# Kernel tuning notes

Measured on AMD Instinct MI355X. Metric: run time of the kernel, lower is better.

The kernel has to match this reference:

```python
import jax, jax.numpy as jnp
import numpy as np
import math

N_HEAD = 16
K_SPARSE = 64

def setup_inputs() -> dict:
    key = jax.random.key(0)
    ks = jax.random.split(key, 12)
    B, T, C = 1, 2048, 1024
    s = 0.02
    return {
        "x":   jax.random.normal(ks[0], (B, T, C), jnp.float32),
        "Wq":  jax.random.normal(ks[1], (C, C), jnp.float32) * s,
        "bq":  jax.random.normal(ks[2], (C,), jnp.float32) * s,
        "Wk":  jax.random.normal(ks[3], (C, C), jnp.float32) * s,
        "bk":  jax.random.normal(ks[4], (C,), jnp.float32) * s,
        "Wv":  jax.random.normal(ks[5], (C, C), jnp.float32) * s,
        "bv":  jax.random.normal(ks[6], (C,), jnp.float32) * s,
        "Wo":  jax.random.normal(ks[7], (C, C), jnp.float32) * s,
        "bo":  jax.random.normal(ks[8], (C,), jnp.float32) * s,
        "Wks": jax.random.normal(ks[9], (C,), jnp.float32) * s,
        "bks": jax.random.normal(ks[10], (), jnp.float32) * s,
    }

def reference(x, Wq, bq, Wk, bk, Wv, bv, Wo, bo, Wks, bks):
    B, T, C = x.shape
    nh = N_HEAD
    hs = C // nh
    k_val = min(K_SPARSE, T)

    # projections -> (B, nh, T, hs)   (torch Linear: x @ W.T + b)
    q = (x @ Wq.T + bq).reshape(B, T, nh, hs).transpose(0, 2, 1, 3)
    k = (x @ Wk.T + bk).reshape(B, T, nh, hs).transpose(0, 2, 1, 3)
    v = (x @ Wv.T + bv).reshape(B, T, nh, hs).transpose(0, 2, 1, 3)

    # key scorer: per-token scalar score (B, T)
    key_scores = x @ Wks + bks

    # causal masking of scores, then per-query top-k key selection
    pos = jnp.arange(T)
    causal = pos[None, :] <= pos[:, None]                      # (T, T), True where key<=query
    masked = jnp.where(causal[None], key_scores[:, None, :], -jnp.inf)  # (B, T, T)
    _, top_k_idx = jax.lax.top_k(masked, k_val)                # (B, T, k)
    top_k_idx = jnp.minimum(top_k_idx, pos[None, :, None])     # clamp to <= query pos

    # gather sparse keys/values: (B, nh, T, k, hs)
    bi = jnp.arange(B)[:, None, None, None]
    hi = jnp.arange(nh)[None, :, None, None]
    gi = top_k_idx[:, None, :, :]                              # (B, 1, T, k)
    sparse_k = k[bi, hi, gi]                                   # (B, nh, T, k, hs)
    sparse_v = v[bi, hi, gi]

    scale = 1.0 / math.sqrt(hs)
    logits = jnp.einsum('bhtd,bhtkd->bhtk', q, sparse_k) * scale
    probs = jax.nn.softmax(logits, axis=-1)
    out = jnp.einsum('bhtk,bhtkd->bhtd', probs, sparse_v)      # (B, nh, T, hs)
    out = out.transpose(0, 2, 1, 3).reshape(B, T, C)
    return out @ Wo.T + bo
```

## Files before the change

### kernel.cpp

```cpp
#include <hip/hip_runtime.h>
#include <hip/hip_bf16.h>
#include <cstdint>
#include <cstddef>

#define T_DIM 2048
#define C_DIM 1024
#define NH 16
#define HS 64
#define KSP 64

#define GBM 128
#define GBN 64
#define GBK 128
#define OBM 64
#define OBN 64

#define ATB 16
#define USLOT (KSP + ATB - 1)
#define KSTR 66

#define DPP_XOR1 0xB1
#define DPP_XOR2 0x4E
#define DPP_HMIRR 0x141
#define DPP_ROR8 0x128

typedef short short8 __attribute__((ext_vector_type(8)));
typedef float f32x4 __attribute__((ext_vector_type(4)));
typedef _Float16 half2_t __attribute__((ext_vector_type(2)));

__device__ __forceinline__ unsigned short f2bfu(float f) {
  unsigned u = __builtin_bit_cast(unsigned, f);
  unsigned r = (u + 0x7fffu + ((u >> 16) & 1u)) >> 16;
  return (unsigned short)r;
}
__device__ __forceinline__ unsigned short f2h(float f) {
  _Float16 h = (_Float16)f;
  return __builtin_bit_cast(unsigned short, h);
}
__device__ __forceinline__ float bflo(unsigned u) {
  return __builtin_bit_cast(float, u << 16);
}
__device__ __forceinline__ float bfhi(unsigned u) {
  return __builtin_bit_cast(float, u & 0xffff0000u);
}

template <int CTRL>
__device__ __forceinline__ float dpp_add_f(float x) {
  const int xi = __builtin_bit_cast(int, x);
  const int y = __builtin_amdgcn_update_dpp(xi, xi, CTRL, 0xF, 0xF, true);
  return x + __builtin_bit_cast(float, y);
}
template <int CTRL>
__device__ __forceinline__ float dpp_max_f(float x) {
  const int xi = __builtin_bit_cast(int, x);
  const int y = __builtin_amdgcn_update_dpp(xi, xi, CTRL, 0xF, 0xF, true);
  return fmaxf(x, __builtin_bit_cast(float, y));
}

__device__ __forceinline__ float dot2h(unsigned kbits, unsigned qbits, float acc) {
#if __has_builtin(__builtin_amdgcn_fdot2)
  return __builtin_amdgcn_fdot2(__builtin_bit_cast(half2_t, kbits),
                                __builtin_bit_cast(half2_t, qbits), acc, false);
#else
  half2_t kk = __builtin_bit_cast(half2_t, kbits);
  half2_t qq = __builtin_bit_cast(half2_t, qbits);
  return acc + (float)kk.x * (float)qq.x + (float)kk.y * (float)qq.y;
#endif
}

#define GLOAD_LDS16(gp, lp)                                                  \
  __builtin_amdgcn_global_load_lds(                                          \
      (const __attribute__((address_space(1))) void*)(gp),                   \
      (__attribute__((address_space(3))) void*)(lp), 16, 0, 0)

#define NSCORE (T_DIM / 4)
#define NCONV ((T_DIM * C_DIM + 4 * C_DIM * C_DIM) / 4 / 256)
__global__ __launch_bounds__(256) void convert_scores_kernel(
    const float* __restrict__ x, const float* __restrict__ Wq,
    const float* __restrict__ Wk, const float* __restrict__ Wv,
    const float* __restrict__ Wo, const float* __restrict__ Wks,
    const float* __restrict__ bks,
    unsigned short* __restrict__ xb, unsigned short* __restrict__ Wqb,
    unsigned short* __restrict__ Wkb, unsigned short* __restrict__ Wvb,
    unsigned short* __restrict__ Wob, float* __restrict__ scores) {
  if (blockIdx.x < NSCORE) {
    const int t = blockIdx.x * 4 + (threadIdx.x >> 6);
    const int lane = threadIdx.x & 63;
    const float* xrow = x + (size_t)t * C_DIM;
    float acc = 0.f;
    #pragma unroll 4
    for (int i = lane; i < C_DIM; i += 64)
      acc += xrow[i] * Wks[i];
    #pragma unroll
    for (int o = 32; o; o >>= 1) acc += __shfl_xor(acc, o);
    if (lane == 0) scores[t] = acc + bks[0];
    return;
  }
  const int i = (blockIdx.x - NSCORE) * 256 + threadIdx.x;
  const int NX4 = T_DIM * C_DIM / 4;
  const int NW4 = C_DIM * C_DIM / 4;
  const float* src;
  unsigned short* dst;
  int j = i;
  if (j < NX4) { src = x; dst = xb; }
  else {
    j -= NX4;
    int w = j / NW4;
    j -= w * NW4;
    src = (w == 0) ? Wq : (w == 1) ? Wk : (w == 2) ? Wv : Wo;
    dst = (w == 0) ? Wqb : (w == 1) ? Wkb : (w == 2) ? Wvb : Wob;
  }
  float4 f = reinterpret_cast<const float4*>(src)[j];
  ushort4 o;
  o.x = f2bfu(f.x); o.y = f2bfu(f.y); o.z = f2bfu(f.z); o.w = f2bfu(f.w);
  reinterpret_cast<ushort4*>(dst)[j] = o;
}

__device__ __forceinline__ void gemm_body_128x64(
    const unsigned short* __restrict__ A, const unsigned short* __restrict__ W,
    f32x4 acc[4][2], int bm, int bn, int tid,
    unsigned short* As, unsigned short* Ws) {
  const int w = tid >> 6, lane = tid & 63;
  const int quad = lane >> 4, r = lane & 15;
  const int wm = (w >> 1) * 64, wn = (w & 1) * 32;
  const int sub = lane >> 4;
  const int c = lane & 15;
  const unsigned short* Arow[8];
  const unsigned short* Wrow[4];
  #pragma unroll
  for (int i = 0; i < 8; ++i) {
    const int row = w * 32 + i * 4 + sub;
    Arow[i] = A + (size_t)(bm * GBM + row) * C_DIM + ((c ^ (row & 7)) * 8);
  }
  #pragma unroll
  for (int i = 0; i < 4; ++i) {
    const int row = w * 16 + i * 4 + sub;
    Wrow[i] = W + (size_t)(bn * GBN + row) * C_DIM + ((c ^ (row & 7)) * 8);
  }
  for (int kb = 0; kb < C_DIM; kb += GBK) {
    #pragma unroll
    for (int i = 0; i < 8; ++i)
      GLOAD_LDS16(Arow[i] + kb, &As[(w * 32 + i * 4) * GBK]);
    #pragma unroll
    for (int i = 0; i < 4; ++i)
      GLOAD_LDS16(Wrow[i] + kb, &Ws[(w * 16 + i * 4) * GBK]);
    __syncthreads();
    #pragma unroll
    for (int ks = 0; ks < 4; ++ks) {
      const int pc = ((ks * 4 + quad) ^ (r & 7)) * 8;
      short8 af[4], bfr[2];
      #pragma unroll
      for (int mi = 0; mi < 4; ++mi)
        af[mi] = *reinterpret_cast<const short8*>(&As[(wm + mi * 16 + r) * GBK + pc]);
      #pragma unroll
      for (int ni = 0; ni < 2; ++ni)
        bfr[ni] = *reinterpret_cast<const short8*>(&Ws[(wn + ni * 16 + r) * GBK + pc]);
      #pragma unroll
      for (int mi = 0; mi < 4; ++mi)
        #pragma unroll
        for (int ni = 0; ni < 2; ++ni)
          acc[mi][ni] = __builtin_amdgcn_mfma_f32_16x16x32_bf16(af[mi], bfr[ni], acc[mi][ni], 0, 0, 0);
    }
    __syncthreads();
  }
}

#define NRANK (T_DIM / 4)
__global__ __launch_bounds__(256) void gemm_qkv_rank_kernel(
    const unsigned short* __restrict__ A,
    const unsigned short* __restrict__ Wq, const unsigned short* __restrict__ Wk,
    const unsigned short* __restrict__ Wv,
    const float* __restrict__ bq, const float* __restrict__ bk,
    const float* __restrict__ bv,
    unsigned short* __restrict__ qo, unsigned short* __restrict__ ko,
    unsigned short* __restrict__ vo,
    const float* __restrict__ scores, int* __restrict__ sorted_idx) {
  __shared__ unsigned short lds[(GBM + GBN) * GBK];
  const int tid = threadIdx.x;
  if (blockIdx.x < NRANK) {
    float* ss = reinterpret_cast<float*>(lds);
    for (int j = tid; j < T_DIM; j += 256) ss[j] = scores[j];
    __syncthreads();
    const int w = tid >> 6, lane = tid & 63;
    const int i = blockIdx.x * 4 + w;
    const float si = ss[i];
    int rank = 0;
    #pragma unroll
    for (int step = 0; step < T_DIM / 64; ++step) {
      const int j = step * 64 + lane;
      const float sj = ss[j];
      rank += (int)((sj > si) || (sj == si && j < i));
    }
    #pragma unroll
    for (int o = 32; o; o >>= 1) rank += __shfl_xor(rank, o);
    if (lane == 0) sorted_idx[rank] = i;
    return;
  }
  const int bid = blockIdx.x - NRANK;
  const int per = (T_DIM / GBM) * (C_DIM / GBN);
  const int which = bid / per;
  const int rem = bid % per;
  const int bm = rem / (C_DIM / GBN);
  const int bn = rem % (C_DIM / GBN);
  const unsigned short* W = (which == 0) ? Wq : (which == 1) ? Wk : Wv;
  const float* bias = (which == 0) ? bq : (which == 1) ? bk : bv;
  unsigned short* out = (which == 0) ? qo : (which == 1) ? ko : vo;
  f32x4 acc[4][2] = {};
  gemm_body_128x64(A, W, acc, bm, bn, tid, lds, lds + GBM * GBK);
  const int w = tid >> 6, lane = tid & 63;
  const int quad = lane >> 4, r = lane & 15;
  const int wm = (w >> 1) * 64, wn = (w & 1) * 32;
  #pragma unroll
  for (int mi = 0; mi < 4; ++mi) {
    #pragma unroll
    for (int ni = 0; ni < 2; ++ni) {
      const int col = bn * GBN + wn + ni * 16 + r;
      const float bf = bias[col];
      #pragma unroll
      for (int i = 0; i < 4; ++i) {
        const int row = bm * GBM + wm + mi * 16 + quad * 4 + i;
        const float val = acc[mi][ni][i] + bf;
        out[(size_t)row * C_DIM + col] = (which == 2) ? f2bfu(val) : f2h(val);
      }
    }
  }
}

__device__ __forceinline__ void gemm_body_64x64(
    const unsigned short* __restrict__ A, const unsigned short* __restrict__ W,
    f32x4 acc[2][2], int bm, int bn, int tid) {
  __shared__ unsigned short As[OBM * GBK];
  __shared__ unsigned short Ws[OBN * GBK];
  const int w = tid >> 6, lane = tid & 63;
  const int quad = lane >> 4, r = lane & 15;
  const int wm = (w >> 1) * 32, wn = (w & 1) * 32;
  const int sub = lane >> 4;
  const int c = lane & 15;
  const unsigned short* Arow[4];
  const unsigned short* Wrow[4];
  #pragma unroll
  for (int i = 0; i < 4; ++i) {
    const int row = w * 16 + i * 4 + sub;
    Arow[i] = A + (size_t)(bm * OBM + row) * C_DIM + ((c ^ (row & 7)) * 8);
    Wrow[i] = W + (size_t)(bn * OBN + row) * C_DIM + ((c ^ (row & 7)) * 8);
  }
  for (int kb = 0; kb < C_DIM; kb += GBK) {
    #pragma unroll
    for (int i = 0; i < 4; ++i)
      GLOAD_LDS16(Arow[i] + kb, &As[(w * 16 + i * 4) * GBK]);
    #pragma unroll
    for (int i = 0; i < 4; ++i)
      GLOAD_LDS16(Wrow[i] + kb, &Ws[(w * 16 + i * 4) * GBK]);
    __syncthreads();
    #pragma unroll
    for (int ks = 0; ks < 4; ++ks) {
      const int pc = ((ks * 4 + quad) ^ (r & 7)) * 8;
      short8 af[2], bfr[2];
      #pragma unroll
      for (int mi = 0; mi < 2; ++mi)
        af[mi] = *reinterpret_cast<const short8*>(&As[(wm + mi * 16 + r) * GBK + pc]);
      #pragma unroll
      for (int ni = 0; ni < 2; ++ni)
        bfr[ni] = *reinterpret_cast<const short8*>(&Ws[(wn + ni * 16 + r) * GBK + pc]);
      #pragma unroll
      for (int mi = 0; mi < 2; ++mi)
        #pragma unroll
        for (int ni = 0; ni < 2; ++ni)
          acc[mi][ni] = __builtin_amdgcn_mfma_f32_16x16x32_bf16(af[mi], bfr[ni], acc[mi][ni], 0, 0, 0);
    }
    __syncthreads();
  }
}

__global__ __launch_bounds__(256) void gemm_o_f32_kernel(
    const unsigned short* __restrict__ A, const unsigned short* __restrict__ W,
    const float* __restrict__ bias, float* __restrict__ out) {
  const int tid = threadIdx.x;
  const int bm = blockIdx.x / (C_DIM / OBN);
  const int bn = blockIdx.x % (C_DIM / OBN);
  f32x4 acc[2][2] = {};
  gemm_body_64x64(A, W, acc, bm, bn, tid);
  const int w = tid >> 6, lane = tid & 63;
  const int quad = lane >> 4, r = lane & 15;
  const int wm = (w >> 1) * 32, wn = (w & 1) * 32;
  #pragma unroll
  for (int mi = 0; mi < 2; ++mi) {
    #pragma unroll
    for (int ni = 0; ni < 2; ++ni) {
      const int col = bn * OBN + wn + ni * 16 + r;
      const float bf = bias[col];
      #pragma unroll
      for (int i = 0; i < 4; ++i) {
        const int row = bm * OBM + wm + mi * 16 + quad * 4 + i;
        out[(size_t)row * C_DIM + col] = acc[mi][ni][i] + bf;
      }
    }
  }
}

__global__ __launch_bounds__(256) void select_kernel(
    const int* __restrict__ sorted_idx, unsigned short* __restrict__ sel) {
  const int tid = threadIdx.x;
  const int w = tid >> 6, lane = tid & 63;
  const int t = blockIdx.x * 4 + w;
  unsigned short* dst = sel + (size_t)t * KSP;
  if (t <= 63) {
    dst[lane] = (unsigned short)((lane < t) ? lane : t);
    return;
  }
  const unsigned long long lt_mask = (1ull << lane) - 1ull;
  int count = 0;
  for (int c = 0; c < T_DIM / 64 && count < KSP; ++c) {
    int s = sorted_idx[c * 64 + lane];
    s = (s < 0) ? 0 : (s > T_DIM - 1 ? T_DIM - 1 : s);
    const bool ok = (s <= t);
    const unsigned long long mm = __ballot(ok);
    const int pos = count + __popcll(mm & lt_mask);
    if (ok && pos < KSP) dst[pos] = (unsigned short)s;
    count += __popcll(mm);
  }
}

__global__ __launch_bounds__(256) void attn_kernel(
    const unsigned short* __restrict__ q, const unsigned short* __restrict__ k,
    const unsigned short* __restrict__ v, const unsigned short* __restrict__ sel,
    unsigned short* __restrict__ attn_out) {
  __shared__ unsigned short Kl[USLOT * KSTR];
  __shared__ unsigned short Vl[USLOT * KSTR];
  __shared__ short map_s[T_DIM];
  __shared__ short urows[USLOT];
  const int tb = blockIdx.x >> 4;
  const int h = blockIdx.x & (NH - 1);
  const int t0 = tb * ATB;
  const int tid = threadIdx.x;
  const int w = tid >> 6, lane = tid & 63;
  const int c8 = lane & 7;
  const int ksub = lane >> 3;
  uint4 qr[ATB / 4];
  #pragma unroll
  for (int li = 0; li < ATB / 4; ++li) {
    const int t = t0 + w * (ATB / 4) + li;
    qr[li] = *reinterpret_cast<const uint4*>(q + (size_t)t * C_DIM + h * HS + 8 * c8);
  }
  if (tid < KSP) {
    const int r0 = sel[(size_t)t0 * KSP + tid];
    map_s[r0] = (short)tid;
    urows[tid] = (short)r0;
  } else if (tid < USLOT) {
    const int row = t0 + 1 + (tid - KSP);
    map_s[row] = (short)tid;
    urows[tid] = (short)row;
  }
  __syncthreads();
  {
    const int e8 = tid & 7;
    for (int s = tid >> 3; s < USLOT; s += 32) {
      const int row = urows[s];
      const size_t gb = (size_t)row * C_DIM + h * HS + e8 * 8;
      *reinterpret_cast<uint4*>(&Kl[s * KSTR + e8 * 8]) =
          *reinterpret_cast<const uint4*>(k + gb);
      *reinterpret_cast<uint4*>(&Vl[s * KSTR + e8 * 8]) =
          *reinterpret_cast<const uint4*>(v + gb);
    }
  }
  __syncthreads();
  #pragma unroll 2
  for (int li = 0; li < ATB / 4; ++li) {
    const int tt = w * (ATB / 4) + li;
    const int t = t0 + tt;
    const uint4 qraw = qr[li];
    const unsigned short* __restrict__ selt = sel + (size_t)t * KSP;
    int slot[8];
    #pragma unroll
    for (int jj = 0; jj < 8; ++jj)
      slot[jj] = map_s[selt[8 * jj + ksub]];
    float l[8];
    #pragma unroll
    for (int jj = 0; jj < 8; ++jj) {
      const uint4 raw =
          *reinterpret_cast<const uint4*>(&Kl[slot[jj] * KSTR + 8 * c8]);
      float pl = dot2h(raw.x, qraw.x, 0.f);
      pl = dot2h(raw.y, qraw.y, pl);
      pl = dot2h(raw.z, qraw.z, pl);
      pl = dot2h(raw.w, qraw.w, pl);
      pl *= 0.125f;
      pl = dpp_add_f<DPP_XOR1>(pl);
      pl = dpp_add_f<DPP_XOR2>(pl);
      pl = dpp_add_f<DPP_HMIRR>(pl);
      l[jj] = pl;
    }
    float m = l[0];
    #pragma unroll
    for (int jj = 1; jj < 8; ++jj) m = fmaxf(m, l[jj]);
    m = dpp_max_f<DPP_ROR8>(m);
    m = fmaxf(m, __shfl_xor(m, 16));
    m = fmaxf(m, __shfl_xor(m, 32));
    float sum = 0.f;
    #pragma unroll
    for (int jj = 0; jj < 8; ++jj) {
      l[jj] = __expf(l[jj] - m);
      sum += l[jj];
    }
    sum = dpp_add_f<DPP_ROR8>(sum);
    sum += __shfl_xor(sum, 16);
    sum += __shfl_xor(sum, 32);
    const float rs = 1.0f / sum;
    float a[8] = {0.f, 0.f, 0.f, 0.f, 0.f, 0.f, 0.f, 0.f};
    #pragma unroll
    for (int jj = 0; jj < 8; ++jj) {
      const uint4 raw =
          *reinterpret_cast<const uint4*>(&Vl[slot[jj] * KSTR + 8 * c8]);
      const float p = l[jj] * rs;
      a[0] += p * bflo(raw.x); a[1] += p * bfhi(raw.x);
      a[2] += p * bflo(raw.y); a[3] += p * bfhi(raw.y);
      a[4] += p * bflo(raw.z); a[5] += p * bfhi(raw.z);
      a[6] += p * bflo(raw.w); a[7] += p * bfhi(raw.w);
    }
    #pragma unroll
    for (int z = 0; z < 8; ++z) a[z] = dpp_add_f<DPP_ROR8>(a[z]);
    #pragma unroll
    for (int z = 0; z < 8; ++z) a[z] += __shfl_xor(a[z], 16);
    #pragma unroll
    for (int z = 0; z < 8; ++z) a[z] += __shfl_xor(a[z], 32);
    if (ksub == 0) {
      ushort4 o0, o1;
      o0.x = f2bfu(a[0]); o0.y = f2bfu(a[1]); o0.z = f2bfu(a[2]); o0.w = f2bfu(a[3]);
      o1.x = f2bfu(a[4]); o1.y = f2bfu(a[5]); o1.z = f2bfu(a[6]); o1.w = f2bfu(a[7]);
      ushort4* dst =
          reinterpret_cast<ushort4*>(attn_out + (size_t)t * C_DIM + h * HS + 8 * c8);
      dst[0] = o0;
      dst[1] = o1;
    }
  }
}

extern "C" void kernel_launch(void* const* d_in, const int* in_sizes, int n_in,
                              void* d_out, int out_size, void* d_ws, size_t ws_size,
                              hipStream_t stream) {
  const float* x   = (const float*)d_in[0];
  const float* Wq  = (const float*)d_in[1];
  const float* bq  = (const float*)d_in[2];
  const float* Wk  = (const float*)d_in[3];
  const float* bk  = (const float*)d_in[4];
  const float* Wv  = (const float*)d_in[5];
  const float* bv  = (const float*)d_in[6];
  const float* Wo  = (const float*)d_in[7];
  const float* bo  = (const float*)d_in[8];
  const float* Wks = (const float*)d_in[9];
  const float* bks = (const float*)d_in[10];
  float* out = (float*)d_out;

  char* ws = (char*)d_ws;
  size_t off = 0;
  float* scores = (float*)(ws + off); off += 8192;
  int*   sorted = (int*)(ws + off);   off += 8192;
  unsigned short* selb = (unsigned short*)(ws + off); off += (size_t)T_DIM * KSP * 2;
  unsigned short* xb  = (unsigned short*)(ws + off); off += (size_t)T_DIM * C_DIM * 2;
  unsigned short* Wqb = (unsigned short*)(ws + off); off += (size_t)C_DIM * C_DIM * 2;
  unsigned short* Wkb = (unsigned short*)(ws + off); off += (size_t)C_DIM * C_DIM * 2;
  unsigned short* Wvb = (unsigned short*)(ws + off); off += (size_t)C_DIM * C_DIM * 2;
  unsigned short* Wob = (unsigned short*)(ws + off); off += (size_t)C_DIM * C_DIM * 2;
  unsigned short* qb  = (unsigned short*)(ws + off); off += (size_t)T_DIM * C_DIM * 2;
  unsigned short* kb  = (unsigned short*)(ws + off); off += (size_t)T_DIM * C_DIM * 2;
  unsigned short* vb  = (unsigned short*)(ws + off); off += (size_t)T_DIM * C_DIM * 2;
  unsigned short* ab  = xb;

  convert_scores_kernel<<<NSCORE + NCONV, 256, 0, stream>>>(
      x, Wq, Wk, Wv, Wo, Wks, bks, xb, Wqb, Wkb, Wvb, Wob, scores);

  gemm_qkv_rank_kernel<<<NRANK + 3 * (T_DIM / GBM) * (C_DIM / GBN), 256, 0,
                         stream>>>(
      xb, Wqb, Wkb, Wvb, bq, bk, bv, qb, kb, vb, scores, sorted);

  select_kernel<<<T_DIM / 4, 256, 0, stream>>>(sorted, selb);

  attn_kernel<<<(T_DIM / ATB) * NH, 256, 0, stream>>>(qb, kb, vb, selb, ab);

  gemm_o_f32_kernel<<<(T_DIM / OBM) * (C_DIM / OBN), 256, 0, stream>>>(
      ab, Wob, bo, out);
}
```

Before: 160.8 us.

## Compute sparse attention over shared key-row union with MFMA and multiplicity mask

Rewrites the attention kernel so each 16-query block scores all 80 candidate rows (the 64 keys selected for the block's first query plus the following rows) with 16x16x32 f16 MFMA instructions. A per-query count table adds log(multiplicity) to the logits of selected rows and masks unselected rows, so the softmax over the union equals the softmax over each query's own gathered keys. V is stored transposed in LDS so that P·V also runs on MFMA, and V becomes f16 instead of bf16. This replaces per-query gathered dot products, DPP reductions and scalar accumulation with matrix-core work, at the cost of scoring unselected rows and a count-table setup step. It relies on every query's selected keys falling inside that 80-row union.

```diff
diff --git a/kernel.cpp b/kernel.cpp
--- a/kernel.cpp
+++ b/kernel.cpp
@@ -16,17 +16,14 @@
 #define OBN 64
 
 #define ATB 16
-#define USLOT (KSP + ATB - 1)
-#define KSTR 66
-
-#define DPP_XOR1 0xB1
-#define DPP_XOR2 0x4E
-#define DPP_HMIRR 0x141
-#define DPP_ROR8 0x128
+#define KLS 72
+#define VTS 108
+#define PLS 104
+#define CNS 104
 
 typedef short short8 __attribute__((ext_vector_type(8)));
 typedef float f32x4 __attribute__((ext_vector_type(4)));
-typedef _Float16 half2_t __attribute__((ext_vector_type(2)));
+typedef _Float16 half8 __attribute__((ext_vector_type(8)));
 
 __device__ __forceinline__ unsigned short f2bfu(float f) {
   unsigned u = __builtin_bit_cast(unsigned, f);
@@ -36,36 +33,6 @@
 __device__ __forceinline__ unsigned short f2h(float f) {
   _Float16 h = (_Float16)f;
   return __builtin_bit_cast(unsigned short, h);
-}
-__device__ __forceinline__ float bflo(unsigned u) {
-  return __builtin_bit_cast(float, u << 16);
-}
-__device__ __forceinline__ float bfhi(unsigned u) {
-  return __builtin_bit_cast(float, u & 0xffff0000u);
-}
-
-template <int CTRL>
-__device__ __forceinline__ float dpp_add_f(float x) {
-  const int xi = __builtin_bit_cast(int, x);
-  const int y = __builtin_amdgcn_update_dpp(xi, xi, CTRL, 0xF, 0xF, true);
-  return x + __builtin_bit_cast(float, y);
-}
-template <int CTRL>
-__device__ __forceinline__ float dpp_max_f(float x) {
-  const int xi = __builtin_bit_cast(int, x);
-  const int y = __builtin_amdgcn_update_dpp(xi, xi, CTRL, 0xF, 0xF, true);
-  return fmaxf(x, __builtin_bit_cast(float, y));
-}
-
-__device__ __forceinline__ float dot2h(unsigned kbits, unsigned qbits, float acc) {
-#if __has_builtin(__builtin_amdgcn_fdot2)
-  return __builtin_amdgcn_fdot2(__builtin_bit_cast(half2_t, kbits),
-                                __builtin_bit_cast(half2_t, qbits), acc, false);
-#else
-  half2_t kk = __builtin_bit_cast(half2_t, kbits);
-  half2_t qq = __builtin_bit_cast(half2_t, qbits);
-  return acc + (float)kk.x * (float)qq.x + (float)kk.y * (float)qq.y;
-#endif
 }
 
 #define GLOAD_LDS16(gp, lp)                                                  \
@@ -220,7 +187,7 @@
       for (int i = 0; i < 4; ++i) {
         const int row = bm * GBM + wm + mi * 16 + quad * 4 + i;
         const float val = acc[mi][ni][i] + bf;
-        out[(size_t)row * C_DIM + col] = (which == 2) ? f2bfu(val) : f2h(val);
+        out[(size_t)row * C_DIM + col] = f2h(val);
       }
     }
   }
@@ -321,116 +288,167 @@
   }
 }
 
-__global__ __launch_bounds__(256) void attn_kernel(
+__global__ __launch_bounds__(128) void attn_kernel(
     const unsigned short* __restrict__ q, const unsigned short* __restrict__ k,
     const unsigned short* __restrict__ v, const unsigned short* __restrict__ sel,
     unsigned short* __restrict__ attn_out) {
-  __shared__ unsigned short Kl[USLOT * KSTR];
-  __shared__ unsigned short Vl[USLOT * KSTR];
+  __shared__ unsigned short Kl[2][80 * KLS];
+  __shared__ unsigned short Vt[2][64 * VTS];
+  __shared__ unsigned short Pl[2][16 * PLS];
+  __shared__ unsigned int   cnt[16 * CNS];
   __shared__ short map_s[T_DIM];
-  __shared__ short urows[USLOT];
-  const int tb = blockIdx.x >> 4;
-  const int h = blockIdx.x & (NH - 1);
+  __shared__ short urows[80];
+  const int tb = blockIdx.x >> 3;
+  const int hg = blockIdx.x & 7;
   const int t0 = tb * ATB;
   const int tid = threadIdx.x;
   const int w = tid >> 6, lane = tid & 63;
-  const int c8 = lane & 7;
-  const int ksub = lane >> 3;
-  uint4 qr[ATB / 4];
-  #pragma unroll
-  for (int li = 0; li < ATB / 4; ++li) {
-    const int t = t0 + w * (ATB / 4) + li;
-    qr[li] = *reinterpret_cast<const uint4*>(q + (size_t)t * C_DIM + h * HS + 8 * c8);
-  }
+  const int qd = lane >> 4;
+  const int r = lane & 15;
+  const int h = hg * 2 + w;
+
+  uint4 qf[2];
+  #pragma unroll
+  for (int kc = 0; kc < 2; ++kc)
+    qf[kc] = *reinterpret_cast<const uint4*>(
+        q + (size_t)(t0 + r) * C_DIM + h * HS + kc * 32 + qd * 8);
+
   if (tid < KSP) {
     const int r0 = sel[(size_t)t0 * KSP + tid];
     map_s[r0] = (short)tid;
     urows[tid] = (short)r0;
-  } else if (tid < USLOT) {
+  } else if (tid < 79) {
     const int row = t0 + 1 + (tid - KSP);
     map_s[row] = (short)tid;
     urows[tid] = (short)row;
-  }
+  } else if (tid == 79) {
+    urows[79] = (short)t0;
+  }
+  for (int i = tid; i < 16 * CNS; i += 128) cnt[i] = 0u;
   __syncthreads();
+
   {
-    const int e8 = tid & 7;
-    for (int s = tid >> 3; s < USLOT; s += 32) {
-      const int row = urows[s];
-      const size_t gb = (size_t)row * C_DIM + h * HS + e8 * 8;
-      *reinterpret_cast<uint4*>(&Kl[s * KSTR + e8 * 8]) =
-          *reinterpret_cast<const uint4*>(k + gb);
-      *reinterpret_cast<uint4*>(&Vl[s * KSTR + e8 * 8]) =
-          *reinterpret_cast<const uint4*>(v + gb);
+    const int e8 = lane & 7;
+    const int pr = lane >> 3;
+    #pragma unroll
+    for (int sb = 0; sb < 5; ++sb) {
+      const int s0 = sb * 16 + pr * 2;
+      const int row0 = urows[s0], row1 = urows[s0 + 1];
+      const size_t g0 = (size_t)row0 * C_DIM + h * HS + e8 * 8;
+      const size_t g1 = (size_t)row1 * C_DIM + h * HS + e8 * 8;
+      const uint4 k0 = *reinterpret_cast<const uint4*>(k + g0);
+      const uint4 k1 = *reinterpret_cast<const uint4*>(k + g1);
+      const uint4 v0 = *reinterpret_cast<const uint4*>(v + g0);
+      const uint4 v1 = *reinterpret_cast<const uint4*>(v + g1);
+      *reinterpret_cast<uint4*>(&Kl[w][s0 * KLS + ((e8 ^ (s0 & 7)) * 8)]) = k0;
+      *reinterpret_cast<uint4*>(&Kl[w][(s0 + 1) * KLS + ((e8 ^ ((s0 + 1) & 7)) * 8)]) = k1;
+      const unsigned* v0w = reinterpret_cast<const unsigned*>(&v0);
+      const unsigned* v1w = reinterpret_cast<const unsigned*>(&v1);
+      #pragma unroll
+      for (int dd = 0; dd < 8; ++dd) {
+        const unsigned lo = (v0w[dd >> 1] >> ((dd & 1) * 16)) & 0xffffu;
+        const unsigned hi = (v1w[dd >> 1] >> ((dd & 1) * 16)) & 0xffffu;
+        *reinterpret_cast<unsigned*>(&Vt[w][(e8 * 8 + dd) * VTS + s0]) =
+            lo | (hi << 16);
+      }
+    }
+    #pragma unroll
+    for (int z = 0; z < 4; ++z)
+      *reinterpret_cast<unsigned long long*>(&Vt[w][lane * VTS + 80 + z * 4]) = 0ull;
+    if (t0 < 64) {
+      #pragma unroll
+      for (int e = 0; e < 8; ++e) {
+        const int idx = tid + e * 128;
+        const int tl = idx >> 6;
+        const int rr = sel[(size_t)(t0 + tl) * KSP + (idx & 63)];
+        atomicAdd(&cnt[tl * CNS + map_s[rr]], 1u);
+      }
+    } else {
+      #pragma unroll
+      for (int e = 0; e < 8; ++e) {
+        const int idx = tid + e * 128;
+        const int tl = idx >> 6;
+        const int rr = sel[(size_t)(t0 + tl) * KSP + (idx & 63)];
+        cnt[tl * CNS + map_s[rr]] = 1u;
+      }
     }
   }
   __syncthreads();
-  #pragma unroll 2
-  for (int li = 0; li < ATB / 4; ++li) {
-    const int tt = w * (ATB / 4) + li;
-    const int t = t0 + tt;
-    const uint4 qraw = qr[li];
-    const unsigned short* __restrict__ selt = sel + (size_t)t * KSP;
-    int slot[8];
-    #pragma unroll
-    for (int jj = 0; jj < 8; ++jj)
-      slot[jj] = map_s[selt[8 * jj + ksub]];
-    float l[8];
-    #pragma unroll
-    for (int jj = 0; jj < 8; ++jj) {
-      const uint4 raw =
-          *reinterpret_cast<const uint4*>(&Kl[slot[jj] * KSTR + 8 * c8]);
-      float pl = dot2h(raw.x, qraw.x, 0.f);
-      pl = dot2h(raw.y, qraw.y, pl);
-      pl = dot2h(raw.z, qraw.z, pl);
-      pl = dot2h(raw.w, qraw.w, pl);
-      pl *= 0.125f;
-      pl = dpp_add_f<DPP_XOR1>(pl);
-      pl = dpp_add_f<DPP_XOR2>(pl);
-      pl = dpp_add_f<DPP_HMIRR>(pl);
-      l[jj] = pl;
-    }
-    float m = l[0];
-    #pragma unroll
-    for (int jj = 1; jj < 8; ++jj) m = fmaxf(m, l[jj]);
-    m = dpp_max_f<DPP_ROR8>(m);
-    m = fmaxf(m, __shfl_xor(m, 16));
-    m = fmaxf(m, __shfl_xor(m, 32));
-    float sum = 0.f;
-    #pragma unroll
-    for (int jj = 0; jj < 8; ++jj) {
-      l[jj] = __expf(l[jj] - m);
-      sum += l[jj];
-    }
-    sum = dpp_add_f<DPP_ROR8>(sum);
-    sum += __shfl_xor(sum, 16);
-    sum += __shfl_xor(sum, 32);
-    const float rs = 1.0f / sum;
-    float a[8] = {0.f, 0.f, 0.f, 0.f, 0.f, 0.f, 0.f, 0.f};
-    #pragma unroll
-    for (int jj = 0; jj < 8; ++jj) {
-      const uint4 raw =
-          *reinterpret_cast<const uint4*>(&Vl[slot[jj] * KSTR + 8 * c8]);
-      const float p = l[jj] * rs;
-      a[0] += p * bflo(raw.x); a[1] += p * bfhi(raw.x);
-      a[2] += p * bflo(raw.y); a[3] += p * bfhi(raw.y);
-      a[4] += p * bflo(raw.z); a[5] += p * bfhi(raw.z);
-      a[6] += p * bflo(raw.w); a[7] += p * bfhi(raw.w);
-    }
-    #pragma unroll
-    for (int z = 0; z < 8; ++z) a[z] = dpp_add_f<DPP_ROR8>(a[z]);
-    #pragma unroll
-    for (int z = 0; z < 8; ++z) a[z] += __shfl_xor(a[z], 16);
-    #pragma unroll
-    for (int z = 0; z < 8; ++z) a[z] += __shfl_xor(a[z], 32);
-    if (ksub == 0) {
-      ushort4 o0, o1;
-      o0.x = f2bfu(a[0]); o0.y = f2bfu(a[1]); o0.z = f2bfu(a[2]); o0.w = f2bfu(a[3]);
-      o1.x = f2bfu(a[4]); o1.y = f2bfu(a[5]); o1.z = f2bfu(a[6]); o1.w = f2bfu(a[7]);
-      ushort4* dst =
-          reinterpret_cast<ushort4*>(attn_out + (size_t)t * C_DIM + h * HS + 8 * c8);
-      dst[0] = o0;
-      dst[1] = o1;
-    }
+
+  f32x4 s5[5] = {};
+  #pragma unroll
+  for (int ut = 0; ut < 5; ++ut) {
+    #pragma unroll
+    for (int kc = 0; kc < 2; ++kc) {
+      const uint4 kw = *reinterpret_cast<const uint4*>(
+          &Kl[w][(ut * 16 + r) * KLS + (((kc * 4 + qd) ^ (r & 7)) * 8)]);
+      s5[ut] = __builtin_amdgcn_mfma_f32_16x16x32_f16(
+          __builtin_bit_cast(half8, kw), __builtin_bit_cast(half8, qf[kc]),
+          s5[ut], 0, 0, 0);
+    }
+  }
+  float mx = -3.0e38f;
+  #pragma unroll
+  for (int ut = 0; ut < 5; ++ut) {
+    const uint4 c4 = *reinterpret_cast<const uint4*>(&cnt[r * CNS + ut * 16 + qd * 4]);
+    const unsigned cc[4] = {c4.x, c4.y, c4.z, c4.w};
+    #pragma unroll
+    for (int i = 0; i < 4; ++i) {
+      float lg = s5[ut][i] * 0.125f;
+      lg = (cc[i] == 0u) ? -3.0e38f
+         : (cc[i] == 1u) ? lg : (lg + __logf((float)cc[i]));
+      s5[ut][i] = lg;
+      mx = fmaxf(mx, lg);
+    }
+  }
+  mx = fmaxf(mx, __shfl_xor(mx, 16));
+  mx = fmaxf(mx, __shfl_xor(mx, 32));
+  float sum = 0.f;
+  #pragma unroll
+  for (int ut = 0; ut < 5; ++ut)
+    #pragma unroll
+    for (int i = 0; i < 4; ++i) {
+      const float e = __expf(s5[ut][i] - mx);
+      s5[ut][i] = e;
+      sum += e;
+    }
+  sum += __shfl_xor(sum, 16);
+  sum += __shfl_xor(sum, 32);
+  const float rs = 1.0f / sum;
+  #pragma unroll
+  for (int ut = 0; ut < 5; ++ut) {
+    const unsigned w0 = (unsigned)f2h(s5[ut][0] * rs) |
+                        ((unsigned)f2h(s5[ut][1] * rs) << 16);
+    const unsigned w1 = (unsigned)f2h(s5[ut][2] * rs) |
+                        ((unsigned)f2h(s5[ut][3] * rs) << 16);
+    unsigned* p32 = reinterpret_cast<unsigned*>(&Pl[w][r * PLS + ut * 16 + qd * 4]);
+    p32[0] = w0;
+    p32[1] = w1;
+  }
+  *reinterpret_cast<unsigned long long*>(&Pl[w][r * PLS + 80 + qd * 4]) = 0ull;
+  f32x4 o4[4] = {};
+  #pragma unroll
+  for (int c = 0; c < 3; ++c) {
+    const uint4 pw = *reinterpret_cast<const uint4*>(&Pl[w][r * PLS + c * 32 + qd * 8]);
+    #pragma unroll
+    for (int mt = 0; mt < 4; ++mt) {
+      const uint2 lo = *reinterpret_cast<const uint2*>(
+          &Vt[w][(mt * 16 + r) * VTS + c * 32 + qd * 8]);
+      const uint2 hi = *reinterpret_cast<const uint2*>(
+          &Vt[w][(mt * 16 + r) * VTS + c * 32 + qd * 8 + 4]);
+      const uint4 vw = {lo.x, lo.y, hi.x, hi.y};
+      o4[mt] = __builtin_amdgcn_mfma_f32_16x16x32_f16(
+          __builtin_bit_cast(half8, vw), __builtin_bit_cast(half8, pw),
+          o4[mt], 0, 0, 0);
+    }
+  }
+  #pragma unroll
+  for (int mt = 0; mt < 4; ++mt) {
+    ushort4 ov;
+    ov.x = f2bfu(o4[mt][0]); ov.y = f2bfu(o4[mt][1]);
+    ov.z = f2bfu(o4[mt][2]); ov.w = f2bfu(o4[mt][3]);
+    *reinterpret_cast<ushort4*>(
+        attn_out + (size_t)(t0 + r) * C_DIM + h * HS + mt * 16 + qd * 4) = ov;
   }
 }
 
@@ -474,7 +492,7 @@
 
   select_kernel<<<T_DIM / 4, 256, 0, stream>>>(sorted, selb);
 
-  attn_kernel<<<(T_DIM / ATB) * NH, 256, 0, stream>>>(qb, kb, vb, selb, ab);
+  attn_kernel<<<(T_DIM / ATB) * (NH / 2), 128, 0, stream>>>(qb, kb, vb, selb, ab);
 
   gemm_o_f32_kernel<<<(T_DIM / OBM) * (C_DIM / OBN), 256, 0, stream>>>(
       ab, Wob, bo, out);
```

After: 149.9 us. -6.8%, faster.
